# Optimization experiments

Measured on AMD Instinct MI355X. Metric: run time of the kernel, lower is better.

The kernel has to match this reference:

```python
import jax, jax.numpy as jnp
import numpy as np

B, L, H, N, NLAYERS = 16, 2048, 256, 64, 4
PRENORM = True


def layer_norm(z, scale, bias, eps=1e-5):
    # z: (B, L, H); normalize over last (feature) axis
    mu = jnp.mean(z, axis=-1, keepdims=True)
    var = jnp.var(z, axis=-1, keepdims=True)
    return (z - mu) * jax.lax.rsqrt(var + eps) * scale + bias


def s4_block(u, log_dt, Alog, Aim, Cre, Cim, D, Wout, bout):
    # u: (B, H, L) -- canonical S4D block: FFT conv + D skip + GELU + GLU linear
    Lq = u.shape[-1]
    dt = jnp.exp(log_dt)[:, None]                      # (H, 1)
    A = -jnp.exp(Alog) + 1j * Aim                      # (H, N)
    C = Cre + 1j * Cim                                 # (H, N)
    dtA = A * dt                                       # (H, N)
    Cd = C * (jnp.exp(dtA) - 1.0) / A                  # ZOH discretization
    vand = jnp.exp(dtA[:, :, None] * jnp.arange(Lq))   # (H, N, L) Vandermonde
    K = 2.0 * jnp.real(jnp.einsum('hn,hnl->hl', Cd, vand))  # (H, L) conv kernel
    n = 2 * Lq
    y = jnp.fft.irfft(jnp.fft.rfft(u, n=n) * jnp.fft.rfft(K, n=n), n=n)[..., :Lq]
    y = y + D[:, None] * u
    y = jax.nn.gelu(y)
    z = jnp.einsum('oh,bhl->bol', Wout, y) + bout[None, :, None]  # (B, 2H, L)
    z1, z2 = jnp.split(z, 2, axis=1)
    return z1 * jax.nn.sigmoid(z2)                     # GLU -> (B, H, L)


def setup_inputs() -> dict:
    key = jax.random.key(0)
    ks = jax.random.split(key, 8)
    x = jax.random.normal(ks[0], (B, L, H), jnp.float32)
    # dt log-uniform in [1e-3, 1e-1]
    log_dt = jnp.log(10.0 ** jax.random.uniform(ks[1], (NLAYERS, H), minval=-3.0, maxval=-1.0)).astype(jnp.float32)
    Alog = jnp.log(0.5 * jnp.ones((NLAYERS, H, N), jnp.float32))
    Aim = jnp.broadcast_to(np.pi * jnp.arange(N, dtype=jnp.float32), (NLAYERS, H, N)).copy()
    Cre = jax.random.normal(ks[2], (NLAYERS, H, N), jnp.float32) * (0.5 ** 0.5)
    Cim = jax.random.normal(ks[3], (NLAYERS, H, N), jnp.float32) * (0.5 ** 0.5)
    D = jax.random.normal(ks[4], (NLAYERS, H), jnp.float32)
    Wout = jax.random.normal(ks[5], (NLAYERS, 2 * H, H), jnp.float32) / jnp.sqrt(jnp.float32(H))
    bout = jnp.zeros((NLAYERS, 2 * H), jnp.float32)
    ln_scale = jnp.ones((NLAYERS, H), jnp.float32)
    ln_bias = jnp.zeros((NLAYERS, H), jnp.float32)
    return dict(x=x, log_dt=log_dt, Alog=Alog, Aim=Aim, Cre=Cre, Cim=Cim, D=D,
                Wout=Wout, bout=bout, ln_scale=ln_scale, ln_bias=ln_bias)


def reference(x, log_dt, Alog, Aim, Cre, Cim, D, Wout, bout, ln_scale, ln_bias):
    # x: (B, L, H); module transposes to (B, H, L) internally
    h = jnp.swapaxes(x, -1, -2)
    for i in range(NLAYERS):
        z = h
        if PRENORM:
            z = jnp.swapaxes(layer_norm(jnp.swapaxes(z, -1, -2), ln_scale[i], ln_bias[i]), -1, -2)
        z = s4_block(z, log_dt[i], Alog[i], Aim[i], Cre[i], Cim[i], D[i], Wout[i], bout[i])
        h = z + h  # dropout is identity in eval mode
        if not PRENORM:
            h = jnp.swapaxes(layer_norm(jnp.swapaxes(h, -1, -2), ln_scale[i], ln_bias[i]), -1, -2)
    return jnp.swapaxes(h, -1, -2)
```

## Files before the change

kernel.cpp:

```cpp
#include <hip/hip_runtime.h>
#include <hip/hip_bf16.h>
#include <math.h>

#define Bq 16
#define Lq 2048
#define Hq 256
#define Nst 64
#define LC 128
#define NC 16
#define NL 4
#define BC 256
#define GK 256
#define SZ ((size_t)Bq * Lq * Hq)

typedef __attribute__((ext_vector_type(8))) short short8;
typedef __attribute__((ext_vector_type(4))) float f32x4;
typedef unsigned short u16;
typedef unsigned int u32;

__device__ __forceinline__ u16 f2b(float x) {
  __hip_bfloat16 b = __float2bfloat16(x);
  u16 u; __builtin_memcpy(&u, &b, 2); return u;
}
__device__ __forceinline__ float b2f(u16 u) {
  u32 t = ((u32)u) << 16; float f; __builtin_memcpy(&f, &t, 4); return f;
}
__device__ __forceinline__ void gload16(const void* g, void* l) {
  __builtin_amdgcn_global_load_lds(
      (const __attribute__((address_space(1))) void*)g,
      (__attribute__((address_space(3))) void*)l, 16, 0, 0);
}

__global__ __launch_bounds__(256) void paramA_k(
    const float* __restrict__ log_dt, const float* __restrict__ Alog,
    const float* __restrict__ Aim, const float* __restrict__ Cre,
    const float* __restrict__ Cim,
    float* __restrict__ wv, float* __restrict__ wLc,
    float* __restrict__ dA, float* __restrict__ Cd) {
  int gi = blockIdx.x * blockDim.x + threadIdx.x;
  if (gi >= NL * Hq * Nst) return;
  int layer = gi >> 14;
  int h = (gi & 16383) >> 6;
  float dt = expf(log_dt[layer * Hq + h]);
  float ar = -expf(Alog[gi]);
  float ai = Aim[gi];
  float dr = ar * dt, di = ai * dt;
  dA[2*gi] = dr; dA[2*gi+1] = di;
  float er = expf(dr); float sn, cs; sincosf(di, &sn, &cs);
  float wr = er * cs, wi = er * sn;
  wv[2*gi] = wr; wv[2*gi+1] = wi;
  float e2 = expf(dr * (float)LC); float sn2, cs2; sincosf(di * (float)LC, &sn2, &cs2);
  wLc[2*gi] = e2 * cs2; wLc[2*gi+1] = e2 * sn2;
  float nr = wr - 1.f, ni = wi;
  float d2 = ar*ar + ai*ai;
  float qr = (nr*ar + ni*ai) / d2;
  float qi = (ni*ar - nr*ai) / d2;
  float cr = Cre[gi], ci = Cim[gi];
  Cd[2*gi]   = cr*qr - ci*qi;
  Cd[2*gi+1] = cr*qi + ci*qr;
}

__global__ __launch_bounds__(64) void paramB_k(
    const float* __restrict__ wv, const float* __restrict__ Cd,
    const float* __restrict__ Dv, float* __restrict__ Kt) {
  int lh = blockIdx.x, n = threadIdx.x;
  int i = lh * Nst + n;
  float wr = wv[2*i], wi = wv[2*i+1];
  float cr = Cd[2*i], ci = Cd[2*i+1];
  float pr = 1.f, pi = 0.f;
  for (int m = 0; m < LC; ++m) {
    float v = 2.f * (cr*pr - ci*pi);
    for (int off = 32; off; off >>= 1) v += __shfl_down(v, off);
    if (n == 0) Kt[lh * LC + m] = v + (m == 0 ? Dv[lh] : 0.f);
    float t = pr*wr - pi*wi;
    pi = fmaf(pr, wi, pi*wr);
    pr = t;
  }
}

__global__ __launch_bounds__(256) void paramM_k(
    const float* __restrict__ dA, const float* __restrict__ Cd,
    const float* __restrict__ Kt, u16* __restrict__ Vb, u16* __restrict__ TRb) {
  int lh = blockIdx.x;
  int wid = threadIdx.x >> 6, lane = threadIdx.x & 63;
  __shared__ float kts[LC];
  if (threadIdx.x < LC) kts[threadIdx.x] = Kt[lh * LC + threadIdx.x];
  __syncthreads();
  if (wid < 2) {
    for (int ro = 0; ro < 64; ++ro) {
      int rr = wid * 64 + ro;
      int n = rr >> 1, im = rr & 1;
      float dr = dA[(lh*Nst+n)*2], di = dA[(lh*Nst+n)*2+1];
      #pragma unroll
      for (int half = 0; half < 2; ++half) {
        int j = lane + half * 64;
        float p = (float)(127 - j);
        float e = expf(dr * p); float sn, cs; sincosf(di * p, &sn, &cs);
        Vb[((size_t)lh * 128 + rr) * 128 + j] = f2b(im ? e * sn : e * cs);
      }
    }
  } else {
    for (int to = 0; to < 64; ++to) {
      int t = (wid - 2) * 64 + to;
      #pragma unroll
      for (int half = 0; half < 2; ++half) {
        int j = lane + half * 64;
        float v = (j <= t) ? kts[t - j] : 0.f;
        TRb[((size_t)lh * 128 + t) * 256 + j] = f2b(v);
      }
      #pragma unroll
      for (int half = 0; half < 2; ++half) {
        int rr = lane + half * 64;
        int n = rr >> 1, im = rr & 1;
        float dr = dA[(lh*Nst+n)*2], di = dA[(lh*Nst+n)*2+1];
        float cr = Cd[(lh*Nst+n)*2], ci = Cd[(lh*Nst+n)*2+1];
        float p = (float)(t + 1);
        float e = expf(dr * p); float sn, cs; sincosf(di * p, &sn, &cs);
        float wpr = e * cs, wpi = e * sn;
        float qr = cr*wpr - ci*wpi, qi = cr*wpi + ci*wpr;
        TRb[((size_t)lh * 128 + t) * 256 + 128 + rr] = f2b(im ? -2.f*qi : 2.f*qr);
      }
    }
  }
}

__global__ __launch_bounds__(256) void cvtw_k(
    const float* __restrict__ w, __hip_bfloat16* __restrict__ wb, int n) {
  int i = blockIdx.x * 256 + threadIdx.x;
  if (i < n) wb[i] = __float2bfloat16(w[i]);
}

__global__ __launch_bounds__(512) void lntr_k(
    const float* __restrict__ src, const float* __restrict__ sc,
    const float* __restrict__ bi, u16* __restrict__ zt) {
  int bc = blockIdx.x, jh = blockIdx.y;
  __shared__ u16 Lt[64][Hq + 6];
  int wave = threadIdx.x >> 6, lane = threadIdx.x & 63;
  float4 scv = ((const float4*)sc)[lane];
  float4 biv = ((const float4*)bi)[lane];
  #pragma unroll
  for (int rr = 0; rr < 8; ++rr) {
    int j = wave * 8 + rr;
    size_t row = (size_t)bc * LC + jh * 64 + j;
    const float4 v = ((const float4*)(src + row * Hq))[lane];
    float s  = v.x + v.y + v.z + v.w;
    float s2 = v.x*v.x + v.y*v.y + v.z*v.z + v.w*v.w;
    for (int off = 32; off; off >>= 1) { s += __shfl_down(s, off); s2 += __shfl_down(s2, off); }
    s = __shfl(s, 0); s2 = __shfl(s2, 0);
    float mu = s * (1.f / Hq);
    float var = s2 * (1.f / Hq) - mu * mu;
    float r = rsqrtf(var + 1e-5f);
    u32 w0 = (u32)f2b((v.x - mu) * r * scv.x + biv.x)
           | ((u32)f2b((v.y - mu) * r * scv.y + biv.y) << 16);
    u32 w1 = (u32)f2b((v.z - mu) * r * scv.z + biv.z)
           | ((u32)f2b((v.w - mu) * r * scv.w + biv.w) << 16);
    *(u32*)&Lt[j][4 * lane]     = w0;
    *(u32*)&Lt[j][4 * lane + 2] = w1;
  }
  __syncthreads();
  #pragma unroll
  for (int it = 0; it < 16; ++it) {
    int idx = it * 512 + threadIdx.x;
    int h = idx >> 5, jl = idx & 31;
    u32 lo = Lt[2*jl][h], hi = Lt[2*jl+1][h];
    ((u32*)zt)[((size_t)h * BC + bc) * 64 + jh * 32 + jl] = lo | (hi << 16);
  }
}

__global__ __launch_bounds__(512) void s4core_k(
    const u16* __restrict__ zt, const u16* __restrict__ Vb,
    const u16* __restrict__ TRb, const float* __restrict__ wLc,
    u16* __restrict__ ytb) {
  int h = blockIdx.y;
  int m0 = blockIdx.x * 128;
  __shared__ u16 As[2][128 * 64];
  __shared__ u16 Bs[128 * 64];
  int tid = threadIdx.x;
  int wid = tid >> 6, lane = tid & 63;
  int cl = lane & 15, kq = lane >> 4;
  int wm = wid & 1, wn = wid >> 1;

  const u16* Ab  = zt  + ((size_t)h * BC + m0) * 128;
  const u16* Vbb = Vb  + (size_t)h * 128 * 128;
  const u16* Tbb = TRb + (size_t)h * 128 * 256;

  #pragma unroll
  for (int half = 0; half < 2; ++half)
    #pragma unroll
    for (int q = 0; q < 2; ++q) {
      int idx = q * 512 + tid;
      int r = idx >> 3, ch = idx & 7;
      gload16(Ab + (size_t)r * 128 + half * 64 + ((ch ^ (r & 7)) << 3),
              (char*)As[half] + (size_t)(q * 512 + (tid & ~63)) * 16);
    }

  auto stageB = [&](const u16* base, int stride, int col0) {
    #pragma unroll
    for (int q = 0; q < 2; ++q) {
      int idx = q * 512 + tid;
      int r = idx >> 3, ch = idx & 7;
      gload16(base + (size_t)r * stride + col0 + ((ch ^ (r & 7)) << 3),
              (char*)Bs + (size_t)(q * 512 + (tid & ~63)) * 16);
    }
  };

  f32x4 accS[4][2] = {};
  f32x4 accY[4][2] = {};

  auto mfstep = [&](const u16* Asrc, f32x4 (*acc)[2]) {
    #pragma unroll
    for (int kk = 0; kk < 2; ++kk) {
      short8 a[4], bf[2];
      #pragma unroll
      for (int mi = 0; mi < 4; ++mi) {
        int m = wm * 64 + mi * 16 + cl;
        int ch = (kk * 4 + kq) ^ (m & 7);
        a[mi] = *(const short8*)(Asrc + m * 64 + ch * 8);
      }
      #pragma unroll
      for (int ni = 0; ni < 2; ++ni) {
        int n = wn * 32 + ni * 16 + cl;
        int ch = (kk * 4 + kq) ^ (n & 7);
        bf[ni] = *(const short8*)(Bs + n * 64 + ch * 8);
      }
      #pragma unroll
      for (int mi = 0; mi < 4; ++mi)
        #pragma unroll
        for (int ni = 0; ni < 2; ++ni)
          acc[mi][ni] = __builtin_amdgcn_mfma_f32_16x16x32_bf16(
              a[mi], bf[ni], acc[mi][ni], 0, 0, 0);
    }
  };

  stageB(Vbb, 128, 0);   __syncthreads();
  mfstep(As[0], accS);   __syncthreads();
  stageB(Vbb, 128, 64);  __syncthreads();
  mfstep(As[1], accS);   __syncthreads();
  stageB(Tbb, 256, 0);   __syncthreads();
  mfstep(As[0], accY);   __syncthreads();
  stageB(Tbb, 256, 64);  __syncthreads();
  mfstep(As[1], accY);

  float sgn = (cl & 1) ? 1.f : -1.f;
  #pragma unroll
  for (int ni = 0; ni < 2; ++ni) {
    int n = (wn * 32 + ni * 16 + cl) >> 1;
    float wr = wLc[2 * (h * Nst + n)];
    float wi = wLc[2 * (h * Nst + n) + 1];
    float swi = sgn * wi;
    #pragma unroll
    for (int mi = 0; mi < 4; ++mi) {
      float carry = 0.f;
      #pragma unroll
      for (int c = 0; c < NC; ++c) {
        float part = __shfl_xor(carry, 1);
        float a_used = accS[mi][ni][c & 3];
        float Sc = fmaf(wr, carry, fmaf(swi, part, a_used));
        if (kq == (c >> 2)) accS[mi][ni][c & 3] = carry;
        carry = __shfl(Sc, ((c >> 2) << 4) + cl);
      }
    }
  }

  __syncthreads();
  #pragma unroll
  for (int mi = 0; mi < 4; ++mi)
    #pragma unroll
    for (int ni = 0; ni < 2; ++ni) {
      int colv = wn * 32 + ni * 16 + cl;
      int half = colv >> 6, cv = colv & 63;
      #pragma unroll
      for (int r = 0; r < 4; ++r) {
        int m = wm * 64 + mi * 16 + kq * 4 + r;
        As[half][m * 64 + (((cv >> 3) ^ (m & 7)) << 3) + (cv & 7)] =
            f2b(accS[mi][ni][r]);
      }
    }
  stageB(Tbb, 256, 128);  __syncthreads();
  mfstep(As[0], accY);    __syncthreads();
  stageB(Tbb, 256, 192);  __syncthreads();
  mfstep(As[1], accY);

  #pragma unroll
  for (int mi = 0; mi < 4; ++mi)
    #pragma unroll
    for (int ni = 0; ni < 2; ++ni) {
      int t = wn * 32 + ni * 16 + cl;
      #pragma unroll
      for (int r = 0; r < 4; ++r) {
        int row = m0 + wm * 64 + mi * 16 + kq * 4 + r;
        float x = accY[mi][ni][r];
        float inner = 0.7978845608028654f * fmaf(0.044715f, x*x*x, x);
        float g = 0.5f * x * (1.f + tanhf(inner));
        ytb[((size_t)h * BC + row) * LC + t] = f2b(g);
      }
    }
}

__global__ __launch_bounds__(256) void trB_k(
    const u16* __restrict__ ytb, u16* __restrict__ ybb) {
  int bc = blockIdx.x;
  int h0 = blockIdx.y * 64;
  __shared__ float Lt[128][65];
  const u16* src = ytb + ((size_t)h0 * BC + bc) * LC;
  for (int it = 0; it < 16; ++it) {
    int idx = it * 256 + threadIdx.x;
    int hh = idx >> 6, tl = idx & 63;
    u32 v = *(const u32*)(src + (size_t)hh * BC * LC + 2 * tl);
    Lt[2*tl][hh]   = b2f((u16)(v & 0xffff));
    Lt[2*tl+1][hh] = b2f((u16)(v >> 16));
  }
  __syncthreads();
  for (int it = 0; it < 16; ++it) {
    int idx = it * 256 + threadIdx.x;
    int t = idx >> 5, hl = idx & 31;
    u32 lo = f2b(Lt[t][2*hl]);
    u32 hi = f2b(Lt[t][2*hl+1]);
    ((u32*)ybb)[((size_t)bc * LC + t) * (Hq / 2) + h0 / 2 + hl] = lo | (hi << 16);
  }
}

__global__ __launch_bounds__(256) void gemm_k(
    const __hip_bfloat16* __restrict__ ybb, const __hip_bfloat16* __restrict__ Wb,
    const float* __restrict__ bout, const float* __restrict__ rsrc,
    float* __restrict__ hb) {
  __shared__ __hip_bfloat16 As[128 * 64];
  __shared__ __hip_bfloat16 Bs[128 * 64];
  int tid = threadIdx.x;
  int m0 = blockIdx.x * 128;
  int ot = blockIdx.y;
  int wid = tid >> 6, lane = tid & 63;
  int cl = lane & 15, kq = lane >> 4;
  f32x4 acc[2][8] = {};
  for (int kt = 0; kt < GK / 64; ++kt) {
    int k0 = kt * 64;
    #pragma unroll
    for (int q = 0; q < 4; ++q) {
      int idx = q * 256 + tid;
      int r = idx >> 3, ch = idx & 7;
      const __hip_bfloat16* sA =
          ybb + (size_t)(m0 + r) * GK + k0 + ((ch ^ (r & 7)) << 3);
      gload16(sA, (char*)As + (size_t)(q * 256 + (tid & ~63)) * 16);
      int wrow = ot * 64 + r + ((r >= 64) ? 192 : 0);
      const __hip_bfloat16* sB =
          Wb + (size_t)wrow * GK + k0 + ((ch ^ (r & 7)) << 3);
      gload16(sB, (char*)Bs + (size_t)(q * 256 + (tid & ~63)) * 16);
    }
    __syncthreads();
    #pragma unroll
    for (int kk = 0; kk < 2; ++kk) {
      short8 a[2], bfr[8];
      #pragma unroll
      for (int mi = 0; mi < 2; ++mi) {
        int m = wid * 32 + mi * 16 + cl;
        int ch = (kk * 4 + kq) ^ (m & 7);
        a[mi] = *(const short8*)(As + m * 64 + ch * 8);
      }
      #pragma unroll
      for (int ni = 0; ni < 8; ++ni) {
        int n = ni * 16 + cl;
        int ch = (kk * 4 + kq) ^ (n & 7);
        bfr[ni] = *(const short8*)(Bs + n * 64 + ch * 8);
      }
      #pragma unroll
      for (int mi = 0; mi < 2; ++mi)
        #pragma unroll
        for (int ni = 0; ni < 8; ++ni)
          acc[mi][ni] = __builtin_amdgcn_mfma_f32_16x16x32_bf16(
              a[mi], bfr[ni], acc[mi][ni], 0, 0, 0);
    }
    __syncthreads();
  }
  #pragma unroll
  for (int mi = 0; mi < 2; ++mi) {
    #pragma unroll
    for (int ni = 0; ni < 4; ++ni) {
      int o1 = ot * 64 + ni * 16 + cl;
      float b1 = bout[o1], b2 = bout[o1 + 256];
      #pragma unroll
      for (int r = 0; r < 4; ++r) {
        int row = m0 + wid * 32 + mi * 16 + kq * 4 + r;
        float z1 = acc[mi][ni][r] + b1;
        float z2 = acc[mi][ni + 4][r] + b2;
        float g = z1 / (1.f + expf(-z2));
        size_t idx = (size_t)row * Hq + o1;
        hb[idx] = rsrc[idx] + g;
      }
    }
  }
}

extern "C" void kernel_launch(void* const* d_in, const int* in_sizes, int n_in,
                              void* d_out, int out_size, void* d_ws, size_t ws_size,
                              hipStream_t stream) {
  (void)in_sizes; (void)n_in; (void)out_size; (void)ws_size;
  const float* x      = (const float*)d_in[0];
  const float* log_dt = (const float*)d_in[1];
  const float* Alog   = (const float*)d_in[2];
  const float* Aim    = (const float*)d_in[3];
  const float* Cre    = (const float*)d_in[4];
  const float* Cim    = (const float*)d_in[5];
  const float* Dv     = (const float*)d_in[6];
  const float* Wout   = (const float*)d_in[7];
  const float* bout   = (const float*)d_in[8];
  const float* lns    = (const float*)d_in[9];
  const float* lnb    = (const float*)d_in[10];

  float* hb = (float*)d_out;
  float* p  = (float*)d_ws;
  u16* zt  = (u16*)p; p += SZ/2;
  u16* ytb = (u16*)p; p += SZ/2;
  u16* ybb = (u16*)p; p += SZ/2;
  u16* Vb  = (u16*)p; p += SZ;
  u16* TRb = (u16*)p; p += 2*SZ;
  u16* Wb  = (u16*)p; p += (NL*2*Hq*Hq)/2;
  float* wv  = p;  p += NL*2*Hq*Nst;
  float* wLc = p;  p += NL*2*Hq*Nst;
  float* dA  = p;  p += NL*2*Hq*Nst;
  float* Cd  = p;  p += NL*2*Hq*Nst;
  float* Kt  = p;  p += NL*Hq*LC;

  cvtw_k<<<(NL*2*Hq*Hq)/256, 256, 0, stream>>>(Wout, (__hip_bfloat16*)Wb, NL*2*Hq*Hq);
  paramA_k<<<(NL*Hq*Nst)/256, 256, 0, stream>>>(
      log_dt, Alog, Aim, Cre, Cim, wv, wLc, dA, Cd);
  paramB_k<<<NL*Hq, 64, 0, stream>>>(wv, Cd, Dv, Kt);
  paramM_k<<<NL*Hq, 256, 0, stream>>>(dA, Cd, Kt, Vb, TRb);

  for (int i = 0; i < NL; ++i) {
    const float* src = (i == 0) ? x : hb;
    lntr_k<<<dim3(BC, 2), 512, 0, stream>>>(src, lns + i*Hq, lnb + i*Hq, zt);
    s4core_k<<<dim3(2, Hq), 512, 0, stream>>>(
        zt, Vb + (size_t)i * Hq * 128 * 128, TRb + (size_t)i * Hq * 128 * 256,
        wLc + (size_t)i * 2 * Hq * Nst, ytb);
    trB_k<<<dim3(BC, 4), 256, 0, stream>>>(ytb, ybb);
    gemm_k<<<dim3((Bq*Lq)/128, 4), 256, 0, stream>>>(
        (const __hip_bfloat16*)ybb,
        (const __hip_bfloat16*)(Wb + (size_t)i * 2 * Hq * Hq),
        bout + (size_t)i*2*Hq, src, hb);
  }
}
```

Baseline: 363.0 us.

## Fuse SSM parameter kernels into one with shared-memory power tables

```diff
diff --git a/kernel.cpp b/kernel.cpp
--- a/kernel.cpp
+++ b/kernel.cpp
@@ -11,6 +11,7 @@
 #define NL 4
 #define BC 256
 #define GK 256
+#define PWS 133
 #define SZ ((size_t)Bq * Lq * Hq)
 
 typedef __attribute__((ext_vector_type(8))) short short8;
@@ -31,96 +32,85 @@
       (__attribute__((address_space(3))) void*)l, 16, 0, 0);
 }
 
-__global__ __launch_bounds__(256) void paramA_k(
+__global__ __launch_bounds__(256) void param_k(
     const float* __restrict__ log_dt, const float* __restrict__ Alog,
     const float* __restrict__ Aim, const float* __restrict__ Cre,
-    const float* __restrict__ Cim,
-    float* __restrict__ wv, float* __restrict__ wLc,
-    float* __restrict__ dA, float* __restrict__ Cd) {
-  int gi = blockIdx.x * blockDim.x + threadIdx.x;
-  if (gi >= NL * Hq * Nst) return;
-  int layer = gi >> 14;
-  int h = (gi & 16383) >> 6;
-  float dt = expf(log_dt[layer * Hq + h]);
-  float ar = -expf(Alog[gi]);
-  float ai = Aim[gi];
-  float dr = ar * dt, di = ai * dt;
-  dA[2*gi] = dr; dA[2*gi+1] = di;
-  float er = expf(dr); float sn, cs; sincosf(di, &sn, &cs);
-  float wr = er * cs, wi = er * sn;
-  wv[2*gi] = wr; wv[2*gi+1] = wi;
-  float e2 = expf(dr * (float)LC); float sn2, cs2; sincosf(di * (float)LC, &sn2, &cs2);
-  wLc[2*gi] = e2 * cs2; wLc[2*gi+1] = e2 * sn2;
-  float nr = wr - 1.f, ni = wi;
-  float d2 = ar*ar + ai*ai;
-  float qr = (nr*ar + ni*ai) / d2;
-  float qi = (ni*ar - nr*ai) / d2;
-  float cr = Cre[gi], ci = Cim[gi];
-  Cd[2*gi]   = cr*qr - ci*qi;
-  Cd[2*gi+1] = cr*qi + ci*qr;
-}
-
-__global__ __launch_bounds__(64) void paramB_k(
-    const float* __restrict__ wv, const float* __restrict__ Cd,
-    const float* __restrict__ Dv, float* __restrict__ Kt) {
-  int lh = blockIdx.x, n = threadIdx.x;
-  int i = lh * Nst + n;
-  float wr = wv[2*i], wi = wv[2*i+1];
-  float cr = Cd[2*i], ci = Cd[2*i+1];
-  float pr = 1.f, pi = 0.f;
-  for (int m = 0; m < LC; ++m) {
-    float v = 2.f * (cr*pr - ci*pi);
-    for (int off = 32; off; off >>= 1) v += __shfl_down(v, off);
-    if (n == 0) Kt[lh * LC + m] = v + (m == 0 ? Dv[lh] : 0.f);
-    float t = pr*wr - pi*wi;
-    pi = fmaf(pr, wi, pi*wr);
-    pr = t;
-  }
-}
-
-__global__ __launch_bounds__(256) void paramM_k(
-    const float* __restrict__ dA, const float* __restrict__ Cd,
-    const float* __restrict__ Kt, u16* __restrict__ Vb, u16* __restrict__ TRb) {
+    const float* __restrict__ Cim, const float* __restrict__ Dv,
+    u16* __restrict__ Vb, u16* __restrict__ TRb, float* __restrict__ wLc) {
   int lh = blockIdx.x;
-  int wid = threadIdx.x >> 6, lane = threadIdx.x & 63;
+  int tid = threadIdx.x;
+  __shared__ float pwre[32][PWS], pwim[32][PWS];
+  __shared__ float cdre[32], cdim[32];
+  __shared__ float kacc[LC];
   __shared__ float kts[LC];
-  if (threadIdx.x < LC) kts[threadIdx.x] = Kt[lh * LC + threadIdx.x];
-  __syncthreads();
-  if (wid < 2) {
-    for (int ro = 0; ro < 64; ++ro) {
-      int rr = wid * 64 + ro;
-      int n = rr >> 1, im = rr & 1;
-      float dr = dA[(lh*Nst+n)*2], di = dA[(lh*Nst+n)*2+1];
-      #pragma unroll
-      for (int half = 0; half < 2; ++half) {
-        int j = lane + half * 64;
-        float p = (float)(127 - j);
-        float e = expf(dr * p); float sn, cs; sincosf(di * p, &sn, &cs);
-        Vb[((size_t)lh * 128 + rr) * 128 + j] = f2b(im ? e * sn : e * cs);
-      }
-    }
-  } else {
-    for (int to = 0; to < 64; ++to) {
-      int t = (wid - 2) * 64 + to;
-      #pragma unroll
-      for (int half = 0; half < 2; ++half) {
-        int j = lane + half * 64;
-        float v = (j <= t) ? kts[t - j] : 0.f;
-        TRb[((size_t)lh * 128 + t) * 256 + j] = f2b(v);
-      }
-      #pragma unroll
-      for (int half = 0; half < 2; ++half) {
-        int rr = lane + half * 64;
-        int n = rr >> 1, im = rr & 1;
-        float dr = dA[(lh*Nst+n)*2], di = dA[(lh*Nst+n)*2+1];
-        float cr = Cd[(lh*Nst+n)*2], ci = Cd[(lh*Nst+n)*2+1];
-        float p = (float)(t + 1);
-        float e = expf(dr * p); float sn, cs; sincosf(di * p, &sn, &cs);
-        float wpr = e * cs, wpi = e * sn;
-        float qr = cr*wpr - ci*wpi, qi = cr*wpi + ci*wpr;
-        TRb[((size_t)lh * 128 + t) * 256 + 128 + rr] = f2b(im ? -2.f*qi : 2.f*qr);
-      }
-    }
+  int ln2 = tid & 31, pg = tid >> 5;
+  float dlt = expf(log_dt[lh]);
+
+  for (int pass = 0; pass < 2; ++pass) {
+    int n = pass * 32 + ln2;
+    int gi = lh * Nst + n;
+    float ar = -expf(Alog[gi]);
+    float ai = Aim[gi];
+    float dr = ar * dlt, di = ai * dlt;
+    float er = expf(dr); float sn, cs; sincosf(di, &sn, &cs);
+    float wr = er * cs, wi = er * sn;
+    float p0 = (float)(16 * pg);
+    float eb = expf(dr * p0); float sb, cb; sincosf(di * p0, &sb, &cb);
+    float pr = eb * cb, pi = eb * sb;
+    #pragma unroll
+    for (int s = 0; s < 16; ++s) {
+      pwre[ln2][16*pg + s] = pr; pwim[ln2][16*pg + s] = pi;
+      float t = pr*wr - pi*wi; pi = fmaf(pr, wi, pi*wr); pr = t;
+    }
+    if (pg == 7) {
+      pwre[ln2][128] = pr; pwim[ln2][128] = pi;
+      wLc[2*gi] = pr; wLc[2*gi+1] = pi;
+    }
+    if (pg == 0) {
+      float nr = wr - 1.f, ni = wi;
+      float d2 = ar*ar + ai*ai;
+      float qr = (nr*ar + ni*ai) / d2;
+      float qi = (ni*ar - nr*ai) / d2;
+      float cr = Cre[gi], ci = Cim[gi];
+      cdre[ln2] = cr*qr - ci*qi;
+      cdim[ln2] = cr*qi + ci*qr;
+    }
+    __syncthreads();
+    if (tid < LC) {
+      float s = 0.f;
+      #pragma unroll
+      for (int k = 0; k < 32; ++k)
+        s = fmaf(cdre[k], pwre[k][tid], fmaf(-cdim[k], pwim[k][tid], s));
+      if (pass == 0) kacc[tid] = s;
+      else kts[tid] = 2.f * (kacc[tid] + s) + ((tid == 0) ? Dv[lh] : 0.f);
+    }
+    #pragma unroll
+    for (int it = 0; it < 32; ++it) {
+      int idx = it * 256 + tid;
+      int rl = idx >> 7, j = idx & 127;
+      int nl = rl >> 1, im = rl & 1;
+      int p = 127 - j;
+      float v = im ? pwim[nl][p] : pwre[nl][p];
+      Vb[((size_t)lh * 128 + 64*pass + rl) * 128 + j] = f2b(v);
+    }
+    #pragma unroll
+    for (int it = 0; it < 32; ++it) {
+      int idx = it * 256 + tid;
+      int t = idx >> 6, rl = idx & 63;
+      int nl = rl >> 1, im = rl & 1;
+      float wpr = pwre[nl][t+1], wpi = pwim[nl][t+1];
+      float qr = cdre[nl]*wpr - cdim[nl]*wpi;
+      float qi = cdre[nl]*wpi + cdim[nl]*wpr;
+      TRb[((size_t)lh * 128 + t) * 256 + 128 + 64*pass + rl] =
+          f2b(im ? -2.f*qi : 2.f*qr);
+    }
+    __syncthreads();
+  }
+  #pragma unroll
+  for (int it = 0; it < 64; ++it) {
+    int idx = it * 256 + tid;
+    int t = idx >> 7, j = idx & 127;
+    TRb[((size_t)lh * 128 + t) * 256 + j] = f2b(j <= t ? kts[t - j] : 0.f);
   }
 }
 
@@ -414,17 +404,10 @@
   u16* Vb  = (u16*)p; p += SZ;
   u16* TRb = (u16*)p; p += 2*SZ;
   u16* Wb  = (u16*)p; p += (NL*2*Hq*Hq)/2;
-  float* wv  = p;  p += NL*2*Hq*Nst;
   float* wLc = p;  p += NL*2*Hq*Nst;
-  float* dA  = p;  p += NL*2*Hq*Nst;
-  float* Cd  = p;  p += NL*2*Hq*Nst;
-  float* Kt  = p;  p += NL*Hq*LC;
 
   cvtw_k<<<(NL*2*Hq*Hq)/256, 256, 0, stream>>>(Wout, (__hip_bfloat16*)Wb, NL*2*Hq*Hq);
-  paramA_k<<<(NL*Hq*Nst)/256, 256, 0, stream>>>(
-      log_dt, Alog, Aim, Cre, Cim, wv, wLc, dA, Cd);
-  paramB_k<<<NL*Hq, 64, 0, stream>>>(wv, Cd, Dv, Kt);
-  paramM_k<<<NL*Hq, 256, 0, stream>>>(dA, Cd, Kt, Vb, TRb);
+  param_k<<<NL*Hq, 256, 0, stream>>>(log_dt, Alog, Aim, Cre, Cim, Dv, Vb, TRb, wLc);
 
   for (int i = 0; i < NL; ++i) {
     const float* src = (i == 0) ? x : hb;
```

New measurement: 306.9 us. 1.18x faster.
